# Kernel tuning notes

Measured on AMD Instinct MI355X. Metric: run time of the kernel, lower is better.

Reference implementation:

```python
import jax, jax.numpy as jnp
import numpy as np

B, C, H, W = 8, 256, 56, 56
R = 2
E = C // R  # embed_dim = in_channels // r


def setup_inputs() -> dict:
    key = jax.random.key(0)
    ks = jax.random.split(key, 10)
    s = 0.02
    return {
        "x": jax.random.normal(ks[0], (B, C, H, W), jnp.float32),
        "Wq": jax.random.normal(ks[1], (E, C), jnp.float32) * s,
        "bq": jax.random.normal(ks[2], (E,), jnp.float32) * s,
        "Wk": jax.random.normal(ks[3], (E, C), jnp.float32) * s,
        "bk": jax.random.normal(ks[4], (E,), jnp.float32) * s,
        "Wv": jax.random.normal(ks[5], (E, C), jnp.float32) * s,
        "bv": jax.random.normal(ks[6], (E,), jnp.float32) * s,
        "Wcat": jax.random.normal(ks[7], (1, 2 * E), jnp.float32) * s,  # 1x1 conv, no bias
        "Wexp": jax.random.normal(ks[8], (C, E), jnp.float32) * s,
        "bexp": jax.random.normal(ks[9], (C,), jnp.float32) * s,
    }


def reference(x, Wq, bq, Wk, bk, Wv, bv, Wcat, Wexp, bexp):
    b, c, h, w = x.shape
    n = h * w
    xf = x.reshape(b, c, n)  # 1x1 convs are channel matmuls over flattened pixels
    q = jnp.einsum('ec,bcn->ben', Wq, xf) + bq[None, :, None]   # [b,E,n]
    k = jnp.einsum('ec,bcn->ben', Wk, xf) + bk[None, :, None]   # [b,E,n]
    v = jnp.einsum('ec,bcn->bne', Wv, xf) + bv[None, None, :]   # [b,n,E]
    # concat_project 1x1 conv on qk=[q;k] repeated along a new n2 axis.
    # NOTE: source repeats BOTH q and k as 'b c n1 -> b c n1 n2', so the score
    # is constant along n2: s[b,n1] = ReLU(wq.q[:,n1] + wk.k[:,n1]).
    wq_c, wk_c = Wcat[0, :E], Wcat[0, E:]
    s = jax.nn.relu(jnp.einsum('e,ben->bn', wq_c, q)
                    + jnp.einsum('e,ben->bn', wk_c, k))         # [b,n]
    attn = jnp.broadcast_to(s[:, :, None], (b, n, n)) / n       # [b,n,n]
    embed = jnp.einsum('bij,bje->bie', attn, v)                 # [b,n,E]
    out = jnp.einsum('ce,bne->bcn', Wexp, embed) + bexp[None, :, None]
    return out.reshape(b, c, h, w) + x
```

## Files before the change

kernel.cpp:

```cpp
#include <hip/hip_runtime.h>

#define CC 256
#define EE 128
#define BB 8
#define NN 3136
#define NN4 784
#define T4 8
#define NTILES 98

__device__ __forceinline__ float waveReduceSum(float v) {
    #pragma unroll
    for (int off = 32; off > 0; off >>= 1) v += __shfl_down(v, off, 64);
    return v;
}

__global__ void __launch_bounds__(256) kA(
        const float* __restrict__ x,
        const float* __restrict__ Wq, const float* __restrict__ bq,
        const float* __restrict__ Wk, const float* __restrict__ bk,
        const float* __restrict__ Wcat,
        float* __restrict__ xbar, float* __restrict__ Ag, float* __restrict__ cstg) {
    const int blk = blockIdx.x;
    const int tid = threadIdx.x;
    if (blk == 0) {
        float a = 0.f;
        #pragma unroll 8
        for (int e = 0; e < EE; e++)
            a += Wcat[e] * Wq[e * CC + tid] + Wcat[EE + e] * Wk[e * CC + tid];
        Ag[tid] = a;
        if (tid < 64) {
            float cp = Wcat[tid] * bq[tid] + Wcat[tid + 64] * bq[tid + 64]
                     + Wcat[EE + tid] * bk[tid] + Wcat[EE + tid + 64] * bk[tid + 64];
            cp = waveReduceSum(cp);
            if (tid == 0) cstg[0] = cp;
        }
    } else {
        const int row = blk - 1;
        const float4* xr = (const float4*)(x + (size_t)row * NN);
        float acc = 0.f;
        for (int i = tid; i < NN4; i += 256) {
            float4 v = xr[i];
            acc += (v.x + v.y) + (v.z + v.w);
        }
        acc = waveReduceSum(acc);
        __shared__ float red[4];
        const int wid = tid >> 6, lane = tid & 63;
        if (lane == 0) red[wid] = acc;
        __syncthreads();
        if (tid == 0)
            xbar[row] = (red[0] + red[1] + red[2] + red[3]) * (1.0f / NN);
    }
}

__global__ void __launch_bounds__(256) kG(
        const float* __restrict__ xbar,
        const float* __restrict__ Wv, const float* __restrict__ bv,
        const float* __restrict__ Wexp, float* __restrict__ gexp) {
    const int b = blockIdx.x;
    const int tid = threadIdx.x;

    __shared__ float xb_s[CC];
    __shared__ float u_part[2][EE];
    __shared__ float u_s[EE];

    xb_s[tid] = xbar[b * CC + tid];
    __syncthreads();

    {
        const int e = tid & 127, h = tid >> 7;
        const float4* wv4 = (const float4*)(Wv + (size_t)e * CC + h * 128);
        const float* xbh = xb_s + h * 128;
        float up = 0.f;
        #pragma unroll
        for (int i = 0; i < 32; i++) {
            float4 w = wv4[i];
            up = fmaf(w.x, xbh[i * 4 + 0], up);
            up = fmaf(w.y, xbh[i * 4 + 1], up);
            up = fmaf(w.z, xbh[i * 4 + 2], up);
            up = fmaf(w.w, xbh[i * 4 + 3], up);
        }
        u_part[h][e] = up;
    }
    __syncthreads();
    if (tid < EE) u_s[tid] = u_part[0][tid] + u_part[1][tid] + bv[tid];
    __syncthreads();

    {
        const float4* we4 = (const float4*)(Wexp + (size_t)tid * EE);
        float g = 0.f;
        #pragma unroll
        for (int i = 0; i < 32; i++) {
            float4 w = we4[i];
            g = fmaf(w.x, u_s[i * 4 + 0], g);
            g = fmaf(w.y, u_s[i * 4 + 1], g);
            g = fmaf(w.z, u_s[i * 4 + 2], g);
            g = fmaf(w.w, u_s[i * 4 + 3], g);
        }
        gexp[b * CC + tid] = g;
    }
}

__global__ void __launch_bounds__(256, 8) kB(
        const float* __restrict__ x, const float* __restrict__ gexp,
        const float* __restrict__ bexp, const float* __restrict__ Ag,
        const float* __restrict__ cstg, float* __restrict__ out) {
    const int b    = blockIdx.x / NTILES;
    const int tile = blockIdx.x - b * NTILES;
    const int tid  = threadIdx.x;
    const int wid = tid >> 6, lane = tid & 63;
    const int i4l = tid & 7, cgr = tid >> 3;

    __shared__ float A_s[CC];
    __shared__ float g_s[CC];
    __shared__ float be_s[CC];
    __shared__ float cv_s;
    __shared__ float4 part2[4][8];
    __shared__ float4 s_s[8];

    A_s[tid]  = Ag[tid];
    g_s[tid]  = gexp[b * CC + tid];
    be_s[tid] = bexp[tid];
    if (tid == 0) cv_s = cstg[0];
    __syncthreads();

    const float4* x4 = (const float4*)x + (size_t)b * CC * NN4 + tile * T4;
    float4*       o4 = (float4*)out     + (size_t)b * CC * NN4 + tile * T4;

    float4 xc[8];
    float4 acc4 = make_float4(0.f, 0.f, 0.f, 0.f);
    #pragma unroll
    for (int j = 0; j < 8; j++) {
        const int c = cgr * 8 + j;
        float4 v = x4[(size_t)c * NN4 + i4l];
        xc[j] = v;
        const float a = A_s[c];
        acc4.x = fmaf(a, v.x, acc4.x);
        acc4.y = fmaf(a, v.y, acc4.y);
        acc4.z = fmaf(a, v.z, acc4.z);
        acc4.w = fmaf(a, v.w, acc4.w);
    }
    #pragma unroll
    for (int m = 8; m <= 32; m <<= 1) {
        acc4.x += __shfl_xor(acc4.x, m, 64);
        acc4.y += __shfl_xor(acc4.y, m, 64);
        acc4.z += __shfl_xor(acc4.z, m, 64);
        acc4.w += __shfl_xor(acc4.w, m, 64);
    }
    if (lane < 8) part2[wid][lane] = acc4;
    __syncthreads();
    if (tid < 8) {
        float4 sum = part2[0][tid];
        #pragma unroll
        for (int w = 1; w < 4; w++) {
            float4 p = part2[w][tid];
            sum.x += p.x; sum.y += p.y; sum.z += p.z; sum.w += p.w;
        }
        const float cv = cv_s;
        float4 s;
        s.x = fmaxf(sum.x + cv, 0.f);
        s.y = fmaxf(sum.y + cv, 0.f);
        s.z = fmaxf(sum.z + cv, 0.f);
        s.w = fmaxf(sum.w + cv, 0.f);
        s_s[tid] = s;
    }
    __syncthreads();

    const float4 sv = s_s[i4l];
    #pragma unroll
    for (int j = 0; j < 8; j++) {
        const int c = cgr * 8 + j;
        const float g  = g_s[c];
        const float be = be_s[c];
        const float4 xv = xc[j];
        float4 o;
        o.x = fmaf(sv.x, g, xv.x) + be;
        o.y = fmaf(sv.y, g, xv.y) + be;
        o.z = fmaf(sv.z, g, xv.z) + be;
        o.w = fmaf(sv.w, g, xv.w) + be;
        o4[(size_t)c * NN4 + i4l] = o;
    }
}

extern "C" void kernel_launch(void* const* d_in, const int* in_sizes, int n_in,
                              void* d_out, int out_size, void* d_ws, size_t ws_size,
                              hipStream_t stream) {
    const float* x    = (const float*)d_in[0];
    const float* Wq   = (const float*)d_in[1];
    const float* bq   = (const float*)d_in[2];
    const float* Wk   = (const float*)d_in[3];
    const float* bk   = (const float*)d_in[4];
    const float* Wv   = (const float*)d_in[5];
    const float* bv   = (const float*)d_in[6];
    const float* Wcat = (const float*)d_in[7];
    const float* Wexp = (const float*)d_in[8];
    const float* bexp = (const float*)d_in[9];
    float* out = (float*)d_out;

    float* ws   = (float*)d_ws;
    float* xbar = ws;
    float* Ag   = ws + 2048;
    float* cstg = ws + 2304;
    float* gexp = ws + 2320;

    kA<<<1 + BB * CC, 256, 0, stream>>>(x, Wq, bq, Wk, bk, Wcat, xbar, Ag, cstg);
    kG<<<BB, 256, 0, stream>>>(xbar, Wv, bv, Wexp, gexp);
    kB<<<BB * NTILES, 256, 0, stream>>>(x, gexp, bexp, Ag, cstg, out);
}
```

Measured before the change: 116.2 us.

## Reduce rows per wavefront, move Ag/cstg setup into kG, prefetch x in kB

```diff
diff --git a/kernel.cpp b/kernel.cpp
--- a/kernel.cpp
+++ b/kernel.cpp
@@ -15,14 +15,38 @@
 }
 
 __global__ void __launch_bounds__(256) kA(
-        const float* __restrict__ x,
+        const float* __restrict__ x, float* __restrict__ xbar) {
+    const int tid  = threadIdx.x;
+    const int wid  = tid >> 6, lane = tid & 63;
+    const int row  = blockIdx.x * 4 + wid;
+    const float4* xr = (const float4*)(x + (size_t)row * NN);
+
+    float acc = 0.f;
+    #pragma unroll
+    for (int k = 0; k < 12; k++) {
+        float4 v = xr[lane + (k << 6)];
+        acc += (v.x + v.y) + (v.z + v.w);
+    }
+    if (lane < 16) {
+        float4 v = xr[768 + lane];
+        acc += (v.x + v.y) + (v.z + v.w);
+    }
+    acc = waveReduceSum(acc);
+    if (lane == 0) xbar[row] = acc * (1.0f / NN);
+}
+
+__global__ void __launch_bounds__(256) kG(
+        const float* __restrict__ xbar,
+        const float* __restrict__ Wv, const float* __restrict__ bv,
+        const float* __restrict__ Wexp,
         const float* __restrict__ Wq, const float* __restrict__ bq,
         const float* __restrict__ Wk, const float* __restrict__ bk,
         const float* __restrict__ Wcat,
-        float* __restrict__ xbar, float* __restrict__ Ag, float* __restrict__ cstg) {
-    const int blk = blockIdx.x;
+        float* __restrict__ gexp, float* __restrict__ Ag, float* __restrict__ cstg) {
+    const int b = blockIdx.x;
     const int tid = threadIdx.x;
-    if (blk == 0) {
+
+    if (b == BB) {
         float a = 0.f;
         #pragma unroll 8
         for (int e = 0; e < EE; e++)
@@ -34,30 +58,8 @@
             cp = waveReduceSum(cp);
             if (tid == 0) cstg[0] = cp;
         }
-    } else {
-        const int row = blk - 1;
-        const float4* xr = (const float4*)(x + (size_t)row * NN);
-        float acc = 0.f;
-        for (int i = tid; i < NN4; i += 256) {
-            float4 v = xr[i];
-            acc += (v.x + v.y) + (v.z + v.w);
-        }
-        acc = waveReduceSum(acc);
-        __shared__ float red[4];
-        const int wid = tid >> 6, lane = tid & 63;
-        if (lane == 0) red[wid] = acc;
-        __syncthreads();
-        if (tid == 0)
-            xbar[row] = (red[0] + red[1] + red[2] + red[3]) * (1.0f / NN);
-    }
-}
-
-__global__ void __launch_bounds__(256) kG(
-        const float* __restrict__ xbar,
-        const float* __restrict__ Wv, const float* __restrict__ bv,
-        const float* __restrict__ Wexp, float* __restrict__ gexp) {
-    const int b = blockIdx.x;
-    const int tid = threadIdx.x;
+        return;
+    }
 
     __shared__ float xb_s[CC];
     __shared__ float u_part[2][EE];
@@ -117,23 +119,24 @@
     __shared__ float4 part2[4][8];
     __shared__ float4 s_s[8];
 
+    const float4* x4 = (const float4*)x + (size_t)b * CC * NN4 + tile * T4;
+    float4*       o4 = (float4*)out     + (size_t)b * CC * NN4 + tile * T4;
+    float4 xc[8];
+    #pragma unroll
+    for (int j = 0; j < 8; j++)
+        xc[j] = x4[(size_t)(cgr * 8 + j) * NN4 + i4l];
+
     A_s[tid]  = Ag[tid];
     g_s[tid]  = gexp[b * CC + tid];
     be_s[tid] = bexp[tid];
     if (tid == 0) cv_s = cstg[0];
     __syncthreads();
 
-    const float4* x4 = (const float4*)x + (size_t)b * CC * NN4 + tile * T4;
-    float4*       o4 = (float4*)out     + (size_t)b * CC * NN4 + tile * T4;
-
-    float4 xc[8];
     float4 acc4 = make_float4(0.f, 0.f, 0.f, 0.f);
     #pragma unroll
     for (int j = 0; j < 8; j++) {
-        const int c = cgr * 8 + j;
-        float4 v = x4[(size_t)c * NN4 + i4l];
-        xc[j] = v;
-        const float a = A_s[c];
+        const float a = A_s[cgr * 8 + j];
+        const float4 v = xc[j];
         acc4.x = fmaf(a, v.x, acc4.x);
         acc4.y = fmaf(a, v.y, acc4.y);
         acc4.z = fmaf(a, v.z, acc4.z);
@@ -202,7 +205,8 @@
     float* cstg = ws + 2304;
     float* gexp = ws + 2320;
 
-    kA<<<1 + BB * CC, 256, 0, stream>>>(x, Wq, bq, Wk, bk, Wcat, xbar, Ag, cstg);
-    kG<<<BB, 256, 0, stream>>>(xbar, Wv, bv, Wexp, gexp);
+    kA<<<512, 256, 0, stream>>>(x, xbar);
+    kG<<<BB + 1, 256, 0, stream>>>(xbar, Wv, bv, Wexp, Wq, bq, Wk, bk, Wcat,
+                                   gexp, Ag, cstg);
     kB<<<BB * NTILES, 256, 0, stream>>>(x, gexp, bexp, Ag, cstg, out);
 }
```

Result: faster. 112.3 us (-3.3%).
